# Optimization experiments

Measured on AMD Instinct MI355X. Metric: run time of the kernel, lower is better.

Reference implementation:

```python
import jax, jax.numpy as jnp
import numpy as np

B, S, D, H = 2, 2048, 1024, 16
HD = D // H  # head_dim = 64

def setup_inputs() -> dict:
    key = jax.random.key(0)
    ks = jax.random.split(key, 11)
    s = 1.0 / np.sqrt(D)
    return {
        "query_input": jax.random.normal(ks[0], (B, S, D), jnp.float32),
        "key_input":   jax.random.normal(ks[1], (B, S, D), jnp.float32),
        "value_input": jax.random.normal(ks[2], (B, S, D), jnp.float32),
        "Wq": jax.random.normal(ks[3], (D, D), jnp.float32) * s,
        "bq": jnp.zeros((D,), jnp.float32),
        "Wk": jax.random.normal(ks[4], (D, D), jnp.float32) * s,
        "bk": jnp.zeros((D,), jnp.float32),
        "Wv": jax.random.normal(ks[5], (D, D), jnp.float32) * s,
        "bv": jnp.zeros((D,), jnp.float32),
        "Wo": jax.random.normal(ks[6], (D, D), jnp.float32) * s,
        "bo": jnp.zeros((D,), jnp.float32),
    }

def _split_heads(x):
    b, s, _ = x.shape
    return x.reshape(b, s, H, HD).transpose(0, 2, 1, 3)  # [B,H,S,HD]

def reference(query_input, key_input, value_input, Wq, bq, Wk, bk, Wv, bv, Wo, bo):
    q = _split_heads(query_input @ Wq + bq)
    k = _split_heads(key_input @ Wk + bk)
    v = _split_heads(value_input @ Wv + bv)
    scores = jnp.einsum('bhqd,bhkd->bhqk', q, k) / jnp.sqrt(jnp.float32(HD))
    attn = jax.nn.softmax(scores, axis=-1)
    out = jnp.einsum('bhqk,bhkd->bhqd', attn, v)
    out = out.transpose(0, 2, 1, 3).reshape(query_input.shape[0], -1, H * HD)
    return out @ Wo + bo
```

## Files before the change

### kernel.cpp

```cpp
#include <hip/hip_runtime.h>
#include <hip/hip_bf16.h>
#include <math.h>

#define B_  2
#define S_  2048
#define D_  1024
#define H_  16
#define HD_ 64

typedef __bf16  bf16x8  __attribute__((ext_vector_type(8)));
typedef float   floatx4 __attribute__((ext_vector_type(4)));

#define MFMA16(a, b, c) __builtin_amdgcn_mfma_f32_16x16x32_bf16((a), (b), (c), 0, 0, 0)

__device__ __forceinline__ void load_lds16(const void* g, void* l) {
    __builtin_amdgcn_global_load_lds(
        (const __attribute__((address_space(1))) unsigned int*)g,
        (__attribute__((address_space(3))) unsigned int*)l, 16, 0, 0);
}

__global__ __launch_bounds__(256) void cast3_bf16_k(
    const float* __restrict__ x0, const float* __restrict__ x1, const float* __restrict__ x2,
    __hip_bfloat16* __restrict__ o0, __hip_bfloat16* __restrict__ o1, __hip_bfloat16* __restrict__ o2)
{
    const int z = blockIdx.y;
    const float* src = (z == 0) ? x0 : (z == 1) ? x1 : x2;
    __hip_bfloat16* dst = (z == 0) ? o0 : (z == 1) ? o1 : o2;
    const int i = blockIdx.x * 256 + threadIdx.x;
    const float4* s4 = (const float4*)src;
    const float4 a = s4[2 * i + 0];
    const float4 b = s4[2 * i + 1];
    union { __hip_bfloat16 h[8]; uint4 v; } p;
    p.h[0] = __float2bfloat16(a.x); p.h[1] = __float2bfloat16(a.y);
    p.h[2] = __float2bfloat16(a.z); p.h[3] = __float2bfloat16(a.w);
    p.h[4] = __float2bfloat16(b.x); p.h[5] = __float2bfloat16(b.y);
    p.h[6] = __float2bfloat16(b.z); p.h[7] = __float2bfloat16(b.w);
    ((uint4*)dst)[i] = p.v;
}

__global__ __launch_bounds__(256) void transpose4_cast_k(
    const float* __restrict__ W0, const float* __restrict__ W1,
    const float* __restrict__ W2, const float* __restrict__ W3,
    __hip_bfloat16* __restrict__ T0, __hip_bfloat16* __restrict__ T1,
    __hip_bfloat16* __restrict__ T2, __hip_bfloat16* __restrict__ T3)
{
    const int z = blockIdx.z;
    const float* W = (z == 0) ? W0 : (z == 1) ? W1 : (z == 2) ? W2 : W3;
    __hip_bfloat16* Wt = (z == 0) ? T0 : (z == 1) ? T1 : (z == 2) ? T2 : T3;

    __shared__ float T[64][65];
    const int t  = threadIdx.x;
    const int n0 = blockIdx.x * 64, k0 = blockIdx.y * 64;
    #pragma unroll
    for (int i = 0; i < 4; ++i) {
        const int u = t + i * 256;
        const int r = u >> 4, c4 = (u & 15) * 4;
        const float4 v = *(const float4*)(W + (size_t)(k0 + r) * D_ + n0 + c4);
        T[r][c4 + 0] = v.x; T[r][c4 + 1] = v.y; T[r][c4 + 2] = v.z; T[r][c4 + 3] = v.w;
    }
    __syncthreads();
    #pragma unroll
    for (int i = 0; i < 4; ++i) {
        const int u = t + i * 256;
        const int n = u >> 4, c4 = (u & 15) * 4;
        union { __hip_bfloat16 h[4]; uint2 v; } p;
        #pragma unroll
        for (int j = 0; j < 4; ++j) p.h[j] = __float2bfloat16(T[c4 + j][n]);
        *(uint2*)(Wt + (size_t)(n0 + n) * D_ + k0 + c4) = p.v;
    }
}

__global__ __launch_bounds__(256) void gemm_qkv_k(
    const __hip_bfloat16* __restrict__ xq, const __hip_bfloat16* __restrict__ xk,
    const __hip_bfloat16* __restrict__ xv,
    const __hip_bfloat16* __restrict__ WqT, const __hip_bfloat16* __restrict__ WkT,
    const __hip_bfloat16* __restrict__ WvT,
    const float* __restrict__ bq, const float* __restrict__ bk, const float* __restrict__ bv,
    __hip_bfloat16* __restrict__ Qh, __hip_bfloat16* __restrict__ Kh,
    __hip_bfloat16* __restrict__ Vt)
{
    constexpr int K = 1024;
    __shared__ __align__(16) short As[4][128][8];
    __shared__ __align__(16) short Bs[4][128][8];

    const int z = blockIdx.z;
    const __hip_bfloat16* A  = (z == 0) ? xq  : (z == 1) ? xk  : xv;
    const __hip_bfloat16* Bt = (z == 0) ? WqT : (z == 1) ? WkT : WvT;
    const float* bias        = (z == 0) ? bq  : (z == 1) ? bk  : bv;

    const int t    = threadIdx.x;
    const int lane = t & 63, w = t >> 6;
    const int quad = lane >> 4, l16 = lane & 15;
    const int m0   = blockIdx.y * 128, n0 = blockIdx.x * 128;
    const int wm   = (w >> 1) * 64,    wn = (w & 1) * 64;

    floatx4 acc[4][4] = {};

    for (int k0 = 0; k0 < K; k0 += 32) {
        #pragma unroll
        for (int i = 0; i < 2; ++i) {
            const int c = t + i * 256;
            const int kq = c >> 7, m = c & 127;
            load_lds16(A + (size_t)(m0 + m) * K + k0 + kq * 8, &As[kq][m][0]);
        }
        #pragma unroll
        for (int i = 0; i < 2; ++i) {
            const int c = t + i * 256;
            const int kq = c >> 7, n = c & 127;
            load_lds16(Bt + (size_t)(n0 + n) * K + k0 + kq * 8, &Bs[kq][n][0]);
        }
        __syncthreads();

        bf16x8 af[4], bfr[4];
        #pragma unroll
        for (int mt = 0; mt < 4; ++mt) af[mt]  = *(const bf16x8*)&As[quad][wm + mt * 16 + l16][0];
        #pragma unroll
        for (int nt = 0; nt < 4; ++nt) bfr[nt] = *(const bf16x8*)&Bs[quad][wn + nt * 16 + l16][0];
        #pragma unroll
        for (int mt = 0; mt < 4; ++mt)
            #pragma unroll
            for (int nt = 0; nt < 4; ++nt)
                acc[mt][nt] = MFMA16(af[mt], bfr[nt], acc[mt][nt]);
        __syncthreads();
    }

    const float oscale = (z == 0) ? 0.125f : 1.0f;
    __hip_bfloat16* outp = (z == 0) ? Qh : (z == 1) ? Kh : Vt;

    #pragma unroll
    for (int mt = 0; mt < 4; ++mt)
        #pragma unroll
        for (int nt = 0; nt < 4; ++nt) {
            const int gn = n0 + wn + nt * 16 + l16;
            const float bi = bias[gn];
            #pragma unroll
            for (int r = 0; r < 4; ++r) {
                const int gm = m0 + wm + mt * 16 + quad * 4 + r;
                const float v = (acc[mt][nt][r] + bi) * oscale;
                if (z != 2) {
                    outp[(((size_t)(gm >> 11) * H_ + (gn >> 6)) * S_ + (gm & 2047)) * 64 + (gn & 63)] =
                        __float2bfloat16(v);
                } else {
                    outp[(((size_t)(gm >> 11) * H_ + (gn >> 6)) * 64 + (gn & 63)) * S_ + (gm & 2047)] =
                        __float2bfloat16(v);
                }
            }
        }
}

__global__ __launch_bounds__(256) void gemm_oproj_k(
    const __hip_bfloat16* __restrict__ A, const __hip_bfloat16* __restrict__ Bt,
    const float* __restrict__ bias, float* __restrict__ out)
{
    constexpr int K = 1024, N = 1024;
    __shared__ __align__(16) short As[4][128][8];
    __shared__ __align__(16) short Bs[4][64][8];

    const int t    = threadIdx.x;
    const int lane = t & 63, w = t >> 6;
    const int quad = lane >> 4, l16 = lane & 15;
    const int m0   = blockIdx.y * 128, n0 = blockIdx.x * 64;
    const int wm   = (w >> 1) * 64,    wn = (w & 1) * 32;

    floatx4 acc[4][2] = {};

    for (int k0 = 0; k0 < K; k0 += 32) {
        #pragma unroll
        for (int i = 0; i < 2; ++i) {
            const int c = t + i * 256;
            const int kq = c >> 7, m = c & 127;
            load_lds16(A + (size_t)(m0 + m) * K + k0 + kq * 8, &As[kq][m][0]);
        }
        {
            const int kq = t >> 6, n = t & 63;
            load_lds16(Bt + (size_t)(n0 + n) * K + k0 + kq * 8, &Bs[kq][n][0]);
        }
        __syncthreads();

        bf16x8 af[4], bfr[2];
        #pragma unroll
        for (int mt = 0; mt < 4; ++mt) af[mt]  = *(const bf16x8*)&As[quad][wm + mt * 16 + l16][0];
        #pragma unroll
        for (int nt = 0; nt < 2; ++nt) bfr[nt] = *(const bf16x8*)&Bs[quad][wn + nt * 16 + l16][0];
        #pragma unroll
        for (int mt = 0; mt < 4; ++mt)
            #pragma unroll
            for (int nt = 0; nt < 2; ++nt)
                acc[mt][nt] = MFMA16(af[mt], bfr[nt], acc[mt][nt]);
        __syncthreads();
    }

    #pragma unroll
    for (int mt = 0; mt < 4; ++mt)
        #pragma unroll
        for (int nt = 0; nt < 2; ++nt) {
            const int gn = n0 + wn + nt * 16 + l16;
            const float bi = bias[gn];
            #pragma unroll
            for (int r = 0; r < 4; ++r) {
                const int gm = m0 + wm + mt * 16 + quad * 4 + r;
                out[(size_t)gm * N + gn] = acc[mt][nt][r] + bi;
            }
        }
}

__global__ __launch_bounds__(512) void attn_mfma_k(
    const __hip_bfloat16* __restrict__ Qh, const __hip_bfloat16* __restrict__ Kh,
    const __hip_bfloat16* __restrict__ Vt, __hip_bfloat16* __restrict__ Ctx)
{
    __shared__ __align__(16) short Ks0[8][64][8], Ks1[8][64][8];
    __shared__ __align__(16) short Vs0[8][64][8], Vs1[8][64][8];
    __shared__ __align__(16) __hip_bfloat16 Ps[128][72];

    const int t    = threadIdx.x;
    const int lane = t & 63, w = t >> 6;
    const int quad = lane >> 4, l16 = lane & 15;
    const int b = blockIdx.z, h = blockIdx.y;
    const size_t bh = (size_t)b * H_ + h;
    const int q0 = blockIdx.x * 128;
    const int myrow = w * 16;

    bf16x8 qf[2];
    {
        const __hip_bfloat16* qb = Qh + (bh * S_ + q0 + myrow + l16) * 64;
        qf[0] = *(const bf16x8*)(qb + quad * 8);
        qf[1] = *(const bf16x8*)(qb + 32 + quad * 8);
    }

    floatx4 oacc[4] = {};
    float lsum[4] = {0.f, 0.f, 0.f, 0.f};

    auto stage = [&](int kt, short (*Ks)[64][8], short (*Vs)[64][8]) {
        const int kq = t >> 6, p = t & 63;
        load_lds16(Kh + (bh * S_ + kt * 64 + p) * 64 + kq * 8, &Ks[kq][p][0]);
        load_lds16(Vt + (bh * 64 + p) * S_ + kt * 64 + kq * 8, &Vs[kq][p][0]);
    };

    auto compute = [&](short (*Ks)[64][8], short (*Vs)[64][8]) {
        floatx4 sacc[4] = {};
        #pragma unroll
        for (int ks = 0; ks < 2; ++ks)
            #pragma unroll
            for (int nt = 0; nt < 4; ++nt) {
                const bf16x8 kf = *(const bf16x8*)&Ks[ks * 4 + quad][nt * 16 + l16][0];
                sacc[nt] = MFMA16(qf[ks], kf, sacc[nt]);
            }
        #pragma unroll
        for (int nt = 0; nt < 4; ++nt)
            #pragma unroll
            for (int r = 0; r < 4; ++r) {
                const float p = __expf(sacc[nt][r]);
                lsum[r] += p;
                Ps[myrow + quad * 4 + r][nt * 16 + l16] = __float2bfloat16(p);
            }
        #pragma unroll
        for (int ks = 0; ks < 2; ++ks) {
            const bf16x8 pf = *(const bf16x8*)&Ps[myrow + l16][ks * 32 + quad * 8];
            #pragma unroll
            for (int nt = 0; nt < 4; ++nt) {
                const bf16x8 vf = *(const bf16x8*)&Vs[ks * 4 + quad][nt * 16 + l16][0];
                oacc[nt] = MFMA16(pf, vf, oacc[nt]);
            }
        }
    };

    stage(0, Ks0, Vs0);
    for (int kt = 0; kt < S_ / 64; kt += 2) {
        __syncthreads();
        stage(kt + 1, Ks1, Vs1);
        compute(Ks0, Vs0);
        __syncthreads();
        if (kt + 2 < S_ / 64) stage(kt + 2, Ks0, Vs0);
        compute(Ks1, Vs1);
    }

    #pragma unroll
    for (int off = 1; off < 16; off <<= 1)
        #pragma unroll
        for (int r = 0; r < 4; ++r) lsum[r] += __shfl_xor(lsum[r], off, 64);

    #pragma unroll
    for (int nt = 0; nt < 4; ++nt)
        #pragma unroll
        for (int r = 0; r < 4; ++r) {
            const int qrow = q0 + myrow + quad * 4 + r;
            Ctx[((size_t)b * S_ + qrow) * D_ + h * 64 + nt * 16 + l16] =
                __float2bfloat16(oacc[nt][r] / lsum[r]);
        }
}

extern "C" void kernel_launch(void* const* d_in, const int* in_sizes, int n_in,
                              void* d_out, int out_size, void* d_ws, size_t ws_size,
                              hipStream_t stream)
{
    const float* xq = (const float*)d_in[0];
    const float* xk = (const float*)d_in[1];
    const float* xv = (const float*)d_in[2];
    const float* Wq = (const float*)d_in[3];
    const float* bq = (const float*)d_in[4];
    const float* Wk = (const float*)d_in[5];
    const float* bk = (const float*)d_in[6];
    const float* Wv = (const float*)d_in[7];
    const float* bv = (const float*)d_in[8];
    const float* Wo = (const float*)d_in[9];
    const float* bo = (const float*)d_in[10];
    float* out = (float*)d_out;

    const size_t n = (size_t)B_ * S_ * D_;
    char* p = (char*)d_ws;
    __hip_bfloat16* xqb = (__hip_bfloat16*)p;            p += n * 2;
    __hip_bfloat16* xkb = (__hip_bfloat16*)p;            p += n * 2;
    __hip_bfloat16* xvb = (__hip_bfloat16*)p;            p += n * 2;
    __hip_bfloat16* WqT = (__hip_bfloat16*)p;            p += (size_t)D_ * D_ * 2;
    __hip_bfloat16* WkT = (__hip_bfloat16*)p;            p += (size_t)D_ * D_ * 2;
    __hip_bfloat16* WvT = (__hip_bfloat16*)p;            p += (size_t)D_ * D_ * 2;
    __hip_bfloat16* WoT = (__hip_bfloat16*)p;            p += (size_t)D_ * D_ * 2;
    __hip_bfloat16* Qh  = (__hip_bfloat16*)p;            p += n * 2;
    __hip_bfloat16* Kh  = (__hip_bfloat16*)p;            p += n * 2;
    __hip_bfloat16* Vth = (__hip_bfloat16*)p;            p += n * 2;
    __hip_bfloat16* Ctx = (__hip_bfloat16*)p;            p += n * 2;

    cast3_bf16_k<<<dim3((int)(n / 8 / 256), 3), dim3(256), 0, stream>>>(
        xq, xk, xv, xqb, xkb, xvb);
    transpose4_cast_k<<<dim3(16, 16, 4), dim3(256), 0, stream>>>(
        Wq, Wk, Wv, Wo, WqT, WkT, WvT, WoT);

    gemm_qkv_k<<<dim3(D_ / 128, (B_ * S_) / 128, 3), dim3(256), 0, stream>>>(
        xqb, xkb, xvb, WqT, WkT, WvT, bq, bk, bv, Qh, Kh, Vth);

    attn_mfma_k<<<dim3(S_ / 128, H_, B_), dim3(512), 0, stream>>>(Qh, Kh, Vth, Ctx);

    gemm_oproj_k<<<dim3(D_ / 64, (B_ * S_) / 128), dim3(256), 0, stream>>>(
        Ctx, WoT, bo, out);
}
```

Baseline: 260.7 us.

## Double-buffer LDS tiles in projection GEMMs and swap grid dimension ordering

Result: faster. 253.4 us (-2.8%).

```diff
diff --git a/kernel.cpp b/kernel.cpp
--- a/kernel.cpp
+++ b/kernel.cpp
@@ -80,8 +80,8 @@
     __hip_bfloat16* __restrict__ Vt)
 {
     constexpr int K = 1024;
-    __shared__ __align__(16) short As[4][128][8];
-    __shared__ __align__(16) short Bs[4][128][8];
+    __shared__ __align__(16) short As0[4][128][8], As1[4][128][8];
+    __shared__ __align__(16) short Bs0[4][128][8], Bs1[4][128][8];
 
     const int z = blockIdx.z;
     const __hip_bfloat16* A  = (z == 0) ? xq  : (z == 1) ? xk  : xv;
@@ -91,12 +91,12 @@
     const int t    = threadIdx.x;
     const int lane = t & 63, w = t >> 6;
     const int quad = lane >> 4, l16 = lane & 15;
-    const int m0   = blockIdx.y * 128, n0 = blockIdx.x * 128;
+    const int m0   = blockIdx.x * 128, n0 = blockIdx.y * 128;
     const int wm   = (w >> 1) * 64,    wn = (w & 1) * 64;
 
     floatx4 acc[4][4] = {};
 
-    for (int k0 = 0; k0 < K; k0 += 32) {
+    auto stage = [&](int k0, short (*As)[128][8], short (*Bs)[128][8]) {
         #pragma unroll
         for (int i = 0; i < 2; ++i) {
             const int c = t + i * 256;
@@ -109,8 +109,9 @@
             const int kq = c >> 7, n = c & 127;
             load_lds16(Bt + (size_t)(n0 + n) * K + k0 + kq * 8, &Bs[kq][n][0]);
         }
-        __syncthreads();
-
+    };
+
+    auto compute = [&](short (*As)[128][8], short (*Bs)[128][8]) {
         bf16x8 af[4], bfr[4];
         #pragma unroll
         for (int mt = 0; mt < 4; ++mt) af[mt]  = *(const bf16x8*)&As[quad][wm + mt * 16 + l16][0];
@@ -121,7 +122,16 @@
             #pragma unroll
             for (int nt = 0; nt < 4; ++nt)
                 acc[mt][nt] = MFMA16(af[mt], bfr[nt], acc[mt][nt]);
-        __syncthreads();
+    };
+
+    stage(0, As0, Bs0);
+    for (int k0 = 0; k0 < K; k0 += 64) {
+        __syncthreads();
+        stage(k0 + 32, As1, Bs1);
+        compute(As0, Bs0);
+        __syncthreads();
+        if (k0 + 64 < K) stage(k0 + 64, As0, Bs0);
+        compute(As1, Bs1);
     }
 
     const float oscale = (z == 0) ? 0.125f : 1.0f;
@@ -153,18 +163,18 @@
     const float* __restrict__ bias, float* __restrict__ out)
 {
     constexpr int K = 1024, N = 1024;
-    __shared__ __align__(16) short As[4][128][8];
-    __shared__ __align__(16) short Bs[4][64][8];
+    __shared__ __align__(16) short As0[4][128][8], As1[4][128][8];
+    __shared__ __align__(16) short Bs0[4][64][8],  Bs1[4][64][8];
 
     const int t    = threadIdx.x;
     const int lane = t & 63, w = t >> 6;
     const int quad = lane >> 4, l16 = lane & 15;
-    const int m0   = blockIdx.y * 128, n0 = blockIdx.x * 64;
+    const int m0   = blockIdx.x * 128, n0 = blockIdx.y * 64;
     const int wm   = (w >> 1) * 64,    wn = (w & 1) * 32;
 
     floatx4 acc[4][2] = {};
 
-    for (int k0 = 0; k0 < K; k0 += 32) {
+    auto stage = [&](int k0, short (*As)[128][8], short (*Bs)[64][8]) {
         #pragma unroll
         for (int i = 0; i < 2; ++i) {
             const int c = t + i * 256;
@@ -175,8 +185,9 @@
             const int kq = t >> 6, n = t & 63;
             load_lds16(Bt + (size_t)(n0 + n) * K + k0 + kq * 8, &Bs[kq][n][0]);
         }
-        __syncthreads();
-
+    };
+
+    auto compute = [&](short (*As)[128][8], short (*Bs)[64][8]) {
         bf16x8 af[4], bfr[2];
         #pragma unroll
         for (int mt = 0; mt < 4; ++mt) af[mt]  = *(const bf16x8*)&As[quad][wm + mt * 16 + l16][0];
@@ -187,7 +198,16 @@
             #pragma unroll
             for (int nt = 0; nt < 2; ++nt)
                 acc[mt][nt] = MFMA16(af[mt], bfr[nt], acc[mt][nt]);
-        __syncthreads();
+    };
+
+    stage(0, As0, Bs0);
+    for (int k0 = 0; k0 < K; k0 += 64) {
+        __syncthreads();
+        stage(k0 + 32, As1, Bs1);
+        compute(As0, Bs0);
+        __syncthreads();
+        if (k0 + 64 < K) stage(k0 + 64, As0, Bs0);
+        compute(As1, Bs1);
     }
 
     #pragma unroll
@@ -215,9 +235,9 @@
     const int t    = threadIdx.x;
     const int lane = t & 63, w = t >> 6;
     const int quad = lane >> 4, l16 = lane & 15;
-    const int b = blockIdx.z, h = blockIdx.y;
+    const int b = blockIdx.z, h = blockIdx.x;
     const size_t bh = (size_t)b * H_ + h;
-    const int q0 = blockIdx.x * 128;
+    const int q0 = blockIdx.y * 128;
     const int myrow = w * 16;
 
     bf16x8 qf[2];
@@ -325,11 +345,11 @@
     transpose4_cast_k<<<dim3(16, 16, 4), dim3(256), 0, stream>>>(
         Wq, Wk, Wv, Wo, WqT, WkT, WvT, WoT);
 
-    gemm_qkv_k<<<dim3(D_ / 128, (B_ * S_) / 128, 3), dim3(256), 0, stream>>>(
+    gemm_qkv_k<<<dim3((B_ * S_) / 128, D_ / 128, 3), dim3(256), 0, stream>>>(
         xqb, xkb, xvb, WqT, WkT, WvT, bq, bk, bv, Qh, Kh, Vth);
 
-    attn_mfma_k<<<dim3(S_ / 128, H_, B_), dim3(512), 0, stream>>>(Qh, Kh, Vth, Ctx);
-
-    gemm_oproj_k<<<dim3(D_ / 64, (B_ * S_) / 128), dim3(256), 0, stream>>>(
+    attn_mfma_k<<<dim3(H_, S_ / 128, B_), dim3(512), 0, stream>>>(Qh, Kh, Vth, Ctx);
+
+    gemm_oproj_k<<<dim3((B_ * S_) / 128, D_ / 64), dim3(256), 0, stream>>>(
         Ctx, WoT, bo, out);
 }
```
